# Kernel optimization log

Measured on AMD Instinct MI355X. Metric: run time of the kernel, lower is better.

Reference implementation:

```python
import jax, jax.numpy as jnp
import numpy as np

DIM = 96
D_STATE = 16
EXPAND = 2
D_INNER = EXPAND * DIM
DT_RANK = (DIM + 15) // 16  # 6
B, H, W = 2, 64, 64
K = 4  # scan directions


def _ln(x, w, b, eps=1e-5):
    mu = x.mean(-1, keepdims=True)
    var = x.var(-1, keepdims=True)
    return (x - mu) / jnp.sqrt(var + eps) * w + b


def setup_inputs() -> dict:
    key = jax.random.key(0)
    ks = jax.random.split(key, 10)
    f = jnp.float32
    x = jax.random.normal(ks[0], (B, H, W, DIM), dtype=f)
    y = jax.random.normal(ks[1], (B, H, W, DIM), dtype=f)
    inp = {
        'x': x,
        'y': y,
        'ln_w': jnp.ones((DIM,), f),
        'ln_b': jnp.zeros((DIM,), f),
        'in_proj_w': jax.random.normal(ks[2], (2 * D_INNER, DIM), f) * 0.05,
        'conv_w': jax.random.normal(ks[3], (D_INNER, 1, 3, 3), f) * 0.1,
        'conv_b': jnp.zeros((D_INNER,), f),
        'x_proj_w': jax.random.normal(ks[4], (K, DT_RANK + 2 * D_STATE, D_INNER), f) * 0.05,
        'dt_w': jax.random.normal(ks[5], (K, D_INNER, DT_RANK), f) * 0.1,
        'dt_b': jax.random.normal(ks[6], (K, D_INNER), f) * 0.1,
        'A_log': jnp.broadcast_to(jnp.log(jnp.arange(1, D_STATE + 1, dtype=f)), (K, D_INNER, D_STATE)),
        'Ds': jnp.ones((K, D_INNER), f),
        'out_norm_w': jnp.ones((D_INNER,), f),
        'out_norm_b': jnp.zeros((D_INNER,), f),
        'out_proj_w': jax.random.normal(ks[7], (DIM, D_INNER), f) * 0.05,
    }
    return inp


def _fwd(x, y, ln_w, ln_b, in_proj_w, conv_w, conv_b, x_proj_w, dt_w, dt_b,
         A_log, Ds, out_norm_w, out_norm_b, out_proj_w):
    Bsz, Hh, Ww, C = x.shape
    Din = conv_w.shape[0]
    N = A_log.shape[-1]
    R = dt_w.shape[-1]
    L = Hh * Ww

    diff = jnp.abs(x - y)                       # TemporalSpectrumBlock abs-diff
    h = _ln(diff, ln_w, ln_b)                   # VSSBlock ln_1
    xz = h @ in_proj_w.T                        # (B,H,W,2*Din)
    xm, z = jnp.split(xz, 2, axis=-1)
    xm = xm.transpose(0, 3, 1, 2)               # (B,Din,H,W)
    xm = jax.lax.conv_general_dilated(
        xm, conv_w, (1, 1), 'SAME', feature_group_count=Din,
        dimension_numbers=('NCHW', 'OIHW', 'NCHW')) + conv_b[None, :, None, None]
    xm = jax.nn.silu(xm)

    # 4-directional sequences (B,4,Din,L)
    x0 = xm.reshape(Bsz, Din, L)
    x1 = xm.transpose(0, 1, 3, 2).reshape(Bsz, Din, L)
    xs = jnp.stack([x0, x1], axis=1)
    xs = jnp.concatenate([xs, jnp.flip(xs, axis=-1)], axis=1)

    x_dbl = jnp.einsum('bkdl,kcd->bkcl', xs, x_proj_w)
    dts, Bs, Cs = jnp.split(x_dbl, [R, R + N], axis=2)   # (B,4,R,L),(B,4,N,L),(B,4,N,L)
    dts = jnp.einsum('bkrl,kdr->bkdl', dts, dt_w)
    delta = jax.nn.softplus(dts + dt_b[None, :, :, None])  # (B,4,Din,L)

    A = -jnp.exp(A_log)                                    # (4,Din,N)
    dA = jnp.exp(delta[..., None] * A[None, :, :, None, :])          # (B,4,Din,L,N)
    dBu = delta[..., None] * Bs.transpose(0, 1, 3, 2)[:, :, None] * xs[..., None]

    dA_t = dA.transpose(3, 0, 1, 2, 4)    # (L,B,4,Din,N)
    dBu_t = dBu.transpose(3, 0, 1, 2, 4)
    C_t = Cs.transpose(3, 0, 1, 2)        # (L,B,4,N)
    h0 = jnp.zeros((Bsz, 4, Din, N), dtype=x.dtype)

    def step(hc, inp):
        a, bu, c = inp
        hc = a * hc + bu
        yv = jnp.einsum('bkdn,bkn->bkd', hc, c)
        return hc, yv

    _, ys = jax.lax.scan(step, h0, (dA_t, dBu_t, C_t))    # (L,B,4,Din)
    ys = ys.transpose(1, 2, 3, 0)                          # (B,4,Din,L)
    out_y = ys + Ds[None, :, :, None] * xs

    inv_y = jnp.flip(out_y[:, 2:4], axis=-1)
    wh_y = out_y[:, 1].reshape(Bsz, Din, Ww, Hh).transpose(0, 1, 3, 2).reshape(Bsz, Din, L)
    invwh_y = inv_y[:, 1].reshape(Bsz, Din, Ww, Hh).transpose(0, 1, 3, 2).reshape(Bsz, Din, L)
    yc = out_y[:, 0] + inv_y[:, 0] + wh_y + invwh_y        # (B,Din,L)
    yc = yc.transpose(0, 2, 1).reshape(Bsz, Hh, Ww, Din)

    yn = _ln(yc, out_norm_w, out_norm_b)
    out = (yn * jax.nn.silu(z)) @ out_proj_w.T
    return diff + out                                      # residual around the block


def reference(x, y, ln_w, ln_b, in_proj_w, conv_w, conv_b, x_proj_w, dt_w, dt_b,
              A_log, Ds, out_norm_w, out_norm_b, out_proj_w):
    return _fwd(x, y, ln_w, ln_b, in_proj_w, conv_w, conv_b, x_proj_w, dt_w, dt_b,
                A_log, Ds, out_norm_w, out_norm_b, out_proj_w)
```

## Files before the change

kernel.cpp:

```cpp
#include <hip/hip_runtime.h>
#include <math.h>

#define DIMC 96
#define DIN  192
#define NST  16
#define RNK  6
#define KD   4
#define HH   64
#define WWD  64
#define LL   4096
#define BB   2
#define NC   128
#define CH   32
#define CPK  48

__device__ __forceinline__ int pos_of(int k, int l) {
    int t = ((l & 63) << 6) | (l >> 6);
    switch (k) {
        case 0: return l;
        case 1: return t;
        case 2: return LL - 1 - l;
        default: return ((((LL-1-l) & 63) << 6) | ((LL-1-l) >> 6));
    }
}

__device__ __forceinline__ float silu_f(float v) {
    return v / (1.f + __expf(-v));
}

__global__ __launch_bounds__(1024) void k1_ln_inproj(
    const float* __restrict__ x, const float* __restrict__ y,
    const float* __restrict__ lnw, const float* __restrict__ lnb,
    const float* __restrict__ Win, const float* __restrict__ Wout,
    const float* __restrict__ xpw,
    float* __restrict__ diff, float* __restrict__ xm, float* __restrict__ zbuf,
    float* __restrict__ wT3, float* __restrict__ WoutT)
{
    __shared__ float hT[96*65];
    __shared__ float ps1[16*64], ps2[16*64];
    __shared__ float mus[64], rss[64];
    int t = threadIdx.x;
    int ptile = blockIdx.x >> 1, cgrp = blockIdx.x & 1;
    int p0 = ptile*64;

    {
        int gid = blockIdx.x*1024 + t;
        if (gid < KD*192*CPK) {
            int kk = gid / (192*CPK); int rem = gid - kk*192*CPK;
            int j = rem / CPK, c = rem - j*CPK;
            float v = 0.f;
            if (c < 16)       v = xpw[((size_t)kk*(RNK+2*NST) + RNK + c)*DIN + j];
            else if (c < 32)  v = xpw[((size_t)kk*(RNK+2*NST) + RNK + NST + (c-16))*DIN + j];
            else if (c < 38)  v = xpw[((size_t)kk*(RNK+2*NST) + (c-32))*DIN + j];
            wT3[gid] = v;
        } else if (gid < KD*192*CPK + 192*96) {
            int i = gid - KD*192*CPK;
            int j = i / 96, o = i - j*96;
            WoutT[i] = Wout[o*192 + j];
        }
    }

    #pragma unroll
    for (int s = 0; s < 6; s++) {
        int i = t + 1024*s;
        float v = fabsf(x[(size_t)p0*96 + i] - y[(size_t)p0*96 + i]);
        if (cgrp == 0) diff[(size_t)p0*96 + i] = v;
        int pos = i / 96, ch = i - pos*96;
        hT[ch*65 + pos] = v;
    }
    __syncthreads();
    {
        int pos = t & 63, part = t >> 6;
        float s1 = 0.f, s2 = 0.f;
        #pragma unroll
        for (int m = 0; m < 6; m++) {
            float v = hT[(part*6 + m)*65 + pos];
            s1 += v; s2 += v*v;
        }
        ps1[part*64 + pos] = s1; ps2[part*64 + pos] = s2;
    }
    __syncthreads();
    if (t < 64) {
        float S1 = 0.f, S2 = 0.f;
        #pragma unroll
        for (int i = 0; i < 16; i++) { S1 += ps1[i*64 + t]; S2 += ps2[i*64 + t]; }
        float mu = S1 * (1.f/96.f);
        float var = S2 * (1.f/96.f) - mu*mu;
        mus[t] = mu; rss[t] = rsqrtf(var + 1e-5f);
    }
    __syncthreads();
    #pragma unroll
    for (int s = 0; s < 6; s++) {
        int i = t + 1024*s;
        int pos = i / 96, ch = i - pos*96;
        hT[ch*65 + pos] = (hT[ch*65 + pos] - mus[pos]) * rss[pos] * lnw[ch] + lnb[ch];
    }
    __syncthreads();

    int w = __builtin_amdgcn_readfirstlane(t >> 6);
    int lane = t & 63;
    int c0 = cgrp*192 + w*12;
    const float* wrows = Win + (size_t)c0*96;
    float acc[12];
    #pragma unroll
    for (int cc = 0; cc < 12; cc++) acc[cc] = 0.f;
    #pragma unroll 2
    for (int j = 0; j < 96; j++) {
        float u = hT[j*65 + lane];
        #pragma unroll
        for (int cc = 0; cc < 12; cc++) acc[cc] += u * wrows[cc*96 + j];
    }
    size_t p = (size_t)(p0 + lane);
    float* dst = (c0 < 192) ? (xm + p*192 + c0) : (zbuf + p*192 + (c0 - 192));
    #pragma unroll
    for (int q = 0; q < 3; q++)
        *(float4*)&dst[4*q] = make_float4(acc[4*q], acc[4*q+1], acc[4*q+2], acc[4*q+3]);
}

__global__ __launch_bounds__(192) void k2_conv(
    const float* __restrict__ xm, const float* __restrict__ cw,
    const float* __restrict__ cb, float* __restrict__ xconv)
{
    int p = blockIdx.x;
    int d = threadIdx.x;
    int b = p >> 12;
    int l = p & (LL - 1);
    int hh = l >> 6, ww = l & 63;
    float acc = cb[d];
    const float* wd = cw + d*9;
    #pragma unroll
    for (int di = -1; di <= 1; di++) {
        int h2 = hh + di;
        if ((unsigned)h2 < HH) {
            #pragma unroll
            for (int dj = -1; dj <= 1; dj++) {
                int w2 = ww + dj;
                if ((unsigned)w2 < WWD)
                    acc += wd[(di+1)*3 + (dj+1)] * xm[((size_t)b*LL + h2*WWD + w2)*DIN + d];
            }
        }
    }
    xconv[(size_t)p*DIN + d] = silu_f(acc);
}

__global__ __launch_bounds__(512) void k3_xproj(
    const float* __restrict__ xconv, const float* __restrict__ wT3,
    float* __restrict__ XDK)
{
    __shared__ float uT[64*192];
    int t = threadIdx.x;
    int ptile = blockIdx.x >> 1, wgrp = blockIdx.x & 1;
    int p0 = ptile*64;

    #pragma unroll
    for (int s = 0; s < 24; s++) {
        int i = t + 512*s;
        int pos = i / 192, ch = i - pos*192;
        int c4 = (ch >> 2) ^ (pos & 7);
        uT[pos*192 + (c4 << 2) + (ch & 3)] = xconv[(size_t)(p0 + pos)*192 + ch];
    }
    __syncthreads();

    int w = __builtin_amdgcn_readfirstlane(t >> 6);
    int slot = wgrp*8 + w;
    int k = slot >> 2, cq = slot & 3;
    int lane = t & 63;
    int c0 = cq*12;
    const float* wp = wT3 + (size_t)k*192*CPK + c0;
    const float* urow = uT + lane*192;
    int sw = lane & 7;
    float acc[12];
    #pragma unroll
    for (int cc = 0; cc < 12; cc++) acc[cc] = 0.f;
    #pragma unroll 4
    for (int j4 = 0; j4 < 48; j4++) {
        float4 u4 = *(const float4*)&urow[((j4 ^ sw) << 2)];
        const float* wrow = wp + (j4*4)*CPK;
        #pragma unroll
        for (int cc = 0; cc < 12; cc++) acc[cc] += u4.x * wrow[cc];
        #pragma unroll
        for (int cc = 0; cc < 12; cc++) acc[cc] += u4.y * wrow[CPK + cc];
        #pragma unroll
        for (int cc = 0; cc < 12; cc++) acc[cc] += u4.z * wrow[2*CPK + cc];
        #pragma unroll
        for (int cc = 0; cc < 12; cc++) acc[cc] += u4.w * wrow[3*CPK + cc];
    }
    int p = p0 + lane;
    int b = p >> 12;
    int s = p & (LL - 1);
    int ts = ((s & 63) << 6) | (s >> 6);
    int l;
    switch (k) {
        case 0: l = s; break;
        case 1: l = ts; break;
        case 2: l = LL - 1 - s; break;
        default: l = LL - 1 - ts; break;
    }
    float* dst = XDK + ((size_t)(b*KD + k)*LL + l)*CPK + c0;
    #pragma unroll
    for (int q = 0; q < 3; q++)
        *(float4*)&dst[4*q] = make_float4(acc[4*q], acc[4*q+1], acc[4*q+2], acc[4*q+3]);
}

__global__ __launch_bounds__(192) void k4_scanA(
    const float* __restrict__ xconv, const float* __restrict__ XDK,
    const float* __restrict__ dtw, const float* __restrict__ dtb,
    const float* __restrict__ A_log,
    float* __restrict__ Sarr, float* __restrict__ Q)
{
    int blk = blockIdx.x;
    int c  = blk & (NC - 1);
    int bk = blk >> 7;
    int k  = bk & 3;
    int b  = bk >> 2;
    int d  = threadIdx.x;
    float dw[RNK];
    #pragma unroll
    for (int r = 0; r < RNK; r++) dw[r] = dtw[((size_t)k*DIN + d)*RNK + r];
    float bias = dtb[k*DIN + d];
    float A[NST];
    #pragma unroll
    for (int n = 0; n < NST; n++) A[n] = -__expf(A_log[((size_t)k*DIN + d)*NST + n]);
    bool fastA = true;
    #pragma unroll
    for (int n = 1; n < NST; n++)
        fastA = fastA && (fabsf(A[n] - (float)(n+1)*A[0]) <= 1e-4f*(float)(n+1));

    float h[NST];
    #pragma unroll
    for (int n = 0; n < NST; n++) h[n] = 0.f;
    float S = 0.f;

    size_t rb = ((size_t)bk*LL + c*CH)*CPK;
    if (fastA) {
        #pragma unroll 2
        for (int step = 0; step < CH; step++) {
            const float* rec = XDK + rb + step*CPK;
            float dl = bias;
            #pragma unroll
            for (int r = 0; r < RNK; r++) dl += rec[32 + r] * dw[r];
            dl = (dl > 20.f) ? dl : __logf(1.f + __expf(dl));
            int l = c*CH + step;
            float uu = xconv[((size_t)b*LL + pos_of(k, l))*DIN + d];
            float du = dl * uu;
            S += dl;
            float e1 = __expf(dl * A[0]);
            float e2 = e1*e1, e4 = e2*e2;
            float p0 = e1, p1 = e2, p2 = e2*e1, p3 = e4;
            #pragma unroll
            for (int g = 0; g < 4; g++) {
                h[4*g+0] = p0*h[4*g+0] + du*rec[4*g+0];
                h[4*g+1] = p1*h[4*g+1] + du*rec[4*g+1];
                h[4*g+2] = p2*h[4*g+2] + du*rec[4*g+2];
                h[4*g+3] = p3*h[4*g+3] + du*rec[4*g+3];
                if (g < 3) { p0 *= e4; p1 *= e4; p2 *= e4; p3 *= e4; }
            }
        }
    } else {
        #pragma unroll 2
        for (int step = 0; step < CH; step++) {
            const float* rec = XDK + rb + step*CPK;
            float dl = bias;
            #pragma unroll
            for (int r = 0; r < RNK; r++) dl += rec[32 + r] * dw[r];
            dl = (dl > 20.f) ? dl : __logf(1.f + __expf(dl));
            int l = c*CH + step;
            float uu = xconv[((size_t)b*LL + pos_of(k, l))*DIN + d];
            float du = dl * uu;
            S += dl;
            #pragma unroll
            for (int n = 0; n < NST; n++) {
                float a = __expf(dl * A[n]);
                h[n] = a*h[n] + du*rec[n];
            }
        }
    }
    Sarr[(size_t)blk*DIN + d] = S;
    size_t qb = (size_t)blk*NST*DIN + d;
    #pragma unroll
    for (int n = 0; n < NST; n++) Q[qb + n*DIN] = h[n];
}

__global__ __launch_bounds__(256) void k5_scanB(
    const float* __restrict__ A_log, const float* __restrict__ Sarr,
    float* __restrict__ Q)
{
    int idx = blockIdx.x*256 + threadIdx.x;
    if (idx >= BB*KD*NST*DIN) return;
    int d = idx % DIN;
    int rest = idx / DIN;
    int n = rest % NST; rest /= NST;
    int k = rest & 3;
    int b = rest >> 2;
    int bk = b*KD + k;
    float A = -__expf(A_log[((size_t)k*DIN + d)*NST + n]);
    size_t qstride = (size_t)NST*DIN;
    size_t qbase = (size_t)bk*NC*qstride + n*DIN + d;
    size_t sbase = (size_t)bk*NC*DIN + d;
    float h = 0.f;
    #pragma unroll 4
    for (int c = 0; c < NC; c++) {
        float s = Sarr[sbase + c*DIN];
        float q = Q[qbase + c*qstride];
        Q[qbase + c*qstride] = h;
        h = __expf(A*s)*h + q;
    }
}

__global__ __launch_bounds__(192) void k6_scanC(
    const float* __restrict__ xconv, const float* __restrict__ XDK,
    const float* __restrict__ dtw, const float* __restrict__ dtb,
    const float* __restrict__ A_log, const float* __restrict__ Ds,
    const float* __restrict__ Q, float* __restrict__ outy)
{
    int blk = blockIdx.x;
    int c  = blk & (NC - 1);
    int bk = blk >> 7;
    int k  = bk & 3;
    int b  = bk >> 2;
    int d  = threadIdx.x;
    float dw[RNK];
    #pragma unroll
    for (int r = 0; r < RNK; r++) dw[r] = dtw[((size_t)k*DIN + d)*RNK + r];
    float bias = dtb[k*DIN + d];
    float A[NST];
    #pragma unroll
    for (int n = 0; n < NST; n++) A[n] = -__expf(A_log[((size_t)k*DIN + d)*NST + n]);
    bool fastA = true;
    #pragma unroll
    for (int n = 1; n < NST; n++)
        fastA = fastA && (fabsf(A[n] - (float)(n+1)*A[0]) <= 1e-4f*(float)(n+1));
    float h[NST];
    size_t qb = (size_t)blk*NST*DIN + d;
    #pragma unroll
    for (int n = 0; n < NST; n++) h[n] = Q[qb + n*DIN];
    float Dv = Ds[k*DIN + d];

    size_t rb = ((size_t)bk*LL + c*CH)*CPK;
    if (fastA) {
        #pragma unroll 2
        for (int step = 0; step < CH; step++) {
            const float* rec = XDK + rb + step*CPK;
            float dl = bias;
            #pragma unroll
            for (int r = 0; r < RNK; r++) dl += rec[32 + r] * dw[r];
            dl = (dl > 20.f) ? dl : __logf(1.f + __expf(dl));
            int l = c*CH + step;
            int sp = pos_of(k, l);
            float uu = xconv[((size_t)b*LL + sp)*DIN + d];
            float du = dl * uu;
            float e1 = __expf(dl * A[0]);
            float e2 = e1*e1, e4 = e2*e2;
            float p0 = e1, p1 = e2, p2 = e2*e1, p3 = e4;
            float yv = 0.f;
            #pragma unroll
            for (int g = 0; g < 4; g++) {
                h[4*g+0] = p0*h[4*g+0] + du*rec[4*g+0];
                h[4*g+1] = p1*h[4*g+1] + du*rec[4*g+1];
                h[4*g+2] = p2*h[4*g+2] + du*rec[4*g+2];
                h[4*g+3] = p3*h[4*g+3] + du*rec[4*g+3];
                yv += h[4*g+0]*rec[16+4*g+0] + h[4*g+1]*rec[16+4*g+1]
                    + h[4*g+2]*rec[16+4*g+2] + h[4*g+3]*rec[16+4*g+3];
                if (g < 3) { p0 *= e4; p1 *= e4; p2 *= e4; p3 *= e4; }
            }
            outy[((size_t)bk*LL + sp)*DIN + d] = yv + Dv*uu;
        }
    } else {
        #pragma unroll 2
        for (int step = 0; step < CH; step++) {
            const float* rec = XDK + rb + step*CPK;
            float dl = bias;
            #pragma unroll
            for (int r = 0; r < RNK; r++) dl += rec[32 + r] * dw[r];
            dl = (dl > 20.f) ? dl : __logf(1.f + __expf(dl));
            int l = c*CH + step;
            int sp = pos_of(k, l);
            float uu = xconv[((size_t)b*LL + sp)*DIN + d];
            float du = dl * uu;
            float yv = 0.f;
            #pragma unroll
            for (int n = 0; n < NST; n++) {
                float a = __expf(dl * A[n]);
                h[n] = a*h[n] + du*rec[n];
                yv += h[n] * rec[16 + n];
            }
            outy[((size_t)bk*LL + sp)*DIN + d] = yv + Dv*uu;
        }
    }
}

__global__ __launch_bounds__(512) void k7_out(
    const float* __restrict__ outy, const float* __restrict__ zbuf,
    const float* __restrict__ diff, const float* __restrict__ onw,
    const float* __restrict__ onb, const float* __restrict__ WoutT,
    float* __restrict__ out)
{
    __shared__ float gT[192*65];
    __shared__ float ps1[8*64], ps2[8*64];
    __shared__ float mus[64], rss[64];
    int t = threadIdx.x;
    int ptile = blockIdx.x >> 1, chalf = blockIdx.x & 1;
    int p0 = ptile*64;
    int b = p0 >> 12;
    int l0 = p0 & (LL - 1);
    const size_t seg = (size_t)LL*DIN;
    size_t base = ((size_t)(b*KD)*LL + l0)*DIN;

    #pragma unroll
    for (int s = 0; s < 24; s++) {
        int i = t + 512*s;
        float yc = outy[base + i] + outy[base + seg + i]
                 + outy[base + 2*seg + i] + outy[base + 3*seg + i];
        int pos = i / 192, ch = i - pos*192;
        gT[ch*65 + pos] = yc;
    }
    __syncthreads();
    {
        int pos = t & 63, part = t >> 6;
        float s1 = 0.f, s2 = 0.f;
        #pragma unroll
        for (int m = 0; m < 24; m++) {
            float v = gT[(part*24 + m)*65 + pos];
            s1 += v; s2 += v*v;
        }
        ps1[part*64 + pos] = s1; ps2[part*64 + pos] = s2;
    }
    __syncthreads();
    if (t < 64) {
        float S1 = 0.f, S2 = 0.f;
        #pragma unroll
        for (int i = 0; i < 8; i++) { S1 += ps1[i*64 + t]; S2 += ps2[i*64 + t]; }
        float mu = S1 * (1.f/192.f);
        float var = S2 * (1.f/192.f) - mu*mu;
        mus[t] = mu; rss[t] = rsqrtf(var + 1e-5f);
    }
    __syncthreads();
    #pragma unroll
    for (int s = 0; s < 24; s++) {
        int i = t + 512*s;
        int pos = i / 192, ch = i - pos*192;
        float v = gT[ch*65 + pos];
        float yn = (v - mus[pos]) * rss[pos] * onw[ch] + onb[ch];
        float z = zbuf[(size_t)p0*DIN + i];
        gT[ch*65 + pos] = yn * silu_f(z);
    }
    __syncthreads();

    int w = __builtin_amdgcn_readfirstlane(t >> 6);
    int lane = t & 63;
    int c0 = chalf*48 + w*6;
    const float* wp = WoutT + c0;
    float acc[6];
    #pragma unroll
    for (int cc = 0; cc < 6; cc++) acc[cc] = 0.f;
    #pragma unroll 4
    for (int j = 0; j < 192; j++) {
        float u = gT[j*65 + lane];
        const float* wrow = wp + j*96;
        #pragma unroll
        for (int cc = 0; cc < 6; cc++) acc[cc] += u * wrow[cc];
    }
    size_t p = (size_t)(p0 + lane);
    #pragma unroll
    for (int q = 0; q < 3; q++) {
        float2 dv = *(const float2*)&diff[p*96 + c0 + 2*q];
        *(float2*)&out[p*96 + c0 + 2*q] =
            make_float2(acc[2*q] + dv.x, acc[2*q+1] + dv.y);
    }
}

extern "C" void kernel_launch(void* const* d_in, const int* in_sizes, int n_in,
                              void* d_out, int out_size, void* d_ws, size_t ws_size,
                              hipStream_t stream)
{
    const float* x       = (const float*)d_in[0];
    const float* y       = (const float*)d_in[1];
    const float* ln_w    = (const float*)d_in[2];
    const float* ln_b    = (const float*)d_in[3];
    const float* in_proj = (const float*)d_in[4];
    const float* conv_w  = (const float*)d_in[5];
    const float* conv_b  = (const float*)d_in[6];
    const float* x_proj  = (const float*)d_in[7];
    const float* dt_w    = (const float*)d_in[8];
    const float* dt_b    = (const float*)d_in[9];
    const float* A_log   = (const float*)d_in[10];
    const float* Ds      = (const float*)d_in[11];
    const float* onw     = (const float*)d_in[12];
    const float* onb     = (const float*)d_in[13];
    const float* out_w   = (const float*)d_in[14];
    float* out = (float*)d_out;

    float* ws    = (float*)d_ws;
    float* diff  = ws;
    float* zbuf  = diff  + 786432;
    float* xm    = zbuf  + 1572864;
    float* xconv = xm    + 1572864;
    float* XDK   = xconv + 1572864;
    float* outy  = XDK   + 1572864;
    float* Qbuf  = outy  + 6291456;
    float* Sarr  = Qbuf  + 6291456;
    float* WoutT = Sarr  + 393216;
    float* wT3   = WoutT + 18432;

    const int BL = BB * LL;

    hipLaunchKernelGGL(k1_ln_inproj, dim3(BL/64*2), dim3(1024), 0, stream,
                       x, y, ln_w, ln_b, in_proj, out_w, x_proj,
                       diff, xm, zbuf, wT3, WoutT);
    hipLaunchKernelGGL(k2_conv, dim3(BL), dim3(DIN), 0, stream,
                       xm, conv_w, conv_b, xconv);
    hipLaunchKernelGGL(k3_xproj, dim3(BL/64*2), dim3(512), 0, stream,
                       xconv, wT3, XDK);
    hipLaunchKernelGGL(k4_scanA, dim3(BB*KD*NC), dim3(DIN), 0, stream,
                       xconv, XDK, dt_w, dt_b, A_log, Sarr, Qbuf);
    hipLaunchKernelGGL(k5_scanB, dim3((BB*KD*NST*DIN + 255)/256), dim3(256), 0, stream,
                       A_log, Sarr, Qbuf);
    hipLaunchKernelGGL(k6_scanC, dim3(BB*KD*NC), dim3(DIN), 0, stream,
                       xconv, XDK, dt_w, dt_b, A_log, Ds, Qbuf, outy);
    hipLaunchKernelGGL(k7_out, dim3(BL/64*2), dim3(512), 0, stream,
                       outy, zbuf, diff, onw, onb, WoutT, out);
}
```

Measured before the change: 254.9 us.

## Accumulate four scan directions into one buffer via atomicAdd

The scan output kernel now atomically adds each direction's result into a single combined (B,L,Din) buffer instead of writing four separate per-direction buffers. The extra blocks of the chunk-carry kernel zero that buffer first. The output kernel then reads one value per element instead of summing four. This cuts global write and read traffic and workspace size, at the cost of float atomics with up to four-way contention per address and a non-deterministic summation order.

Measured after the change: 246.1 us, median of 2. -3.5%, faster.

```diff
diff --git a/kernel.cpp b/kernel.cpp
--- a/kernel.cpp
+++ b/kernel.cpp
@@ -13,6 +13,8 @@
 #define NC   128
 #define CH   32
 #define CPK  48
+#define SCANB_BLKS 96
+#define ZERO_BLKS  384
 
 __device__ __forceinline__ int pos_of(int k, int l) {
     int t = ((l & 63) << 6) | (l >> 6);
@@ -283,8 +285,16 @@
 
 __global__ __launch_bounds__(256) void k5_scanB(
     const float* __restrict__ A_log, const float* __restrict__ Sarr,
-    float* __restrict__ Q)
-{
+    float* __restrict__ Q, float* __restrict__ outc)
+{
+    if (blockIdx.x >= SCANB_BLKS) {
+        int zi = (blockIdx.x - SCANB_BLKS)*256 + threadIdx.x;
+        float4* o4 = (float4*)outc;
+        float4 z4 = make_float4(0.f, 0.f, 0.f, 0.f);
+        #pragma unroll
+        for (int j = 0; j < 4; j++) o4[zi + j*98304] = z4;
+        return;
+    }
     int idx = blockIdx.x*256 + threadIdx.x;
     if (idx >= BB*KD*NST*DIN) return;
     int d = idx % DIN;
@@ -311,7 +321,7 @@
     const float* __restrict__ xconv, const float* __restrict__ XDK,
     const float* __restrict__ dtw, const float* __restrict__ dtb,
     const float* __restrict__ A_log, const float* __restrict__ Ds,
-    const float* __restrict__ Q, float* __restrict__ outy)
+    const float* __restrict__ Q, float* __restrict__ outc)
 {
     int blk = blockIdx.x;
     int c  = blk & (NC - 1);
@@ -363,7 +373,7 @@
                     + h[4*g+2]*rec[16+4*g+2] + h[4*g+3]*rec[16+4*g+3];
                 if (g < 3) { p0 *= e4; p1 *= e4; p2 *= e4; p3 *= e4; }
             }
-            outy[((size_t)bk*LL + sp)*DIN + d] = yv + Dv*uu;
+            atomicAdd(&outc[((size_t)b*LL + sp)*DIN + d], yv + Dv*uu);
         }
     } else {
         #pragma unroll 2
@@ -384,13 +394,13 @@
                 h[n] = a*h[n] + du*rec[n];
                 yv += h[n] * rec[16 + n];
             }
-            outy[((size_t)bk*LL + sp)*DIN + d] = yv + Dv*uu;
+            atomicAdd(&outc[((size_t)b*LL + sp)*DIN + d], yv + Dv*uu);
         }
     }
 }
 
 __global__ __launch_bounds__(512) void k7_out(
-    const float* __restrict__ outy, const float* __restrict__ zbuf,
+    const float* __restrict__ outc, const float* __restrict__ zbuf,
     const float* __restrict__ diff, const float* __restrict__ onw,
     const float* __restrict__ onb, const float* __restrict__ WoutT,
     float* __restrict__ out)
@@ -401,16 +411,11 @@
     int t = threadIdx.x;
     int ptile = blockIdx.x >> 1, chalf = blockIdx.x & 1;
     int p0 = ptile*64;
-    int b = p0 >> 12;
-    int l0 = p0 & (LL - 1);
-    const size_t seg = (size_t)LL*DIN;
-    size_t base = ((size_t)(b*KD)*LL + l0)*DIN;
 
     #pragma unroll
     for (int s = 0; s < 24; s++) {
         int i = t + 512*s;
-        float yc = outy[base + i] + outy[base + seg + i]
-                 + outy[base + 2*seg + i] + outy[base + 3*seg + i];
+        float yc = outc[(size_t)p0*DIN + i];
         int pos = i / 192, ch = i - pos*192;
         gT[ch*65 + pos] = yc;
     }
@@ -496,10 +501,10 @@
     float* xm    = zbuf  + 1572864;
     float* xconv = xm    + 1572864;
     float* XDK   = xconv + 1572864;
-    float* outy  = XDK   + 1572864;
-    float* Qbuf  = outy  + 6291456;
-    float* Sarr  = Qbuf  + 6291456;
-    float* WoutT = Sarr  + 393216;
+    float* outc  = XDK   + 1572864;
+    float* Qbuf  = outc  + 1572864;
+    float* Sarr  = Qbuf  + 3145728;
+    float* WoutT = Sarr  + 196608;
     float* wT3   = WoutT + 18432;
 
     const int BL = BB * LL;
@@ -513,10 +518,10 @@
                        xconv, wT3, XDK);
     hipLaunchKernelGGL(k4_scanA, dim3(BB*KD*NC), dim3(DIN), 0, stream,
                        xconv, XDK, dt_w, dt_b, A_log, Sarr, Qbuf);
-    hipLaunchKernelGGL(k5_scanB, dim3((BB*KD*NST*DIN + 255)/256), dim3(256), 0, stream,
-                       A_log, Sarr, Qbuf);
+    hipLaunchKernelGGL(k5_scanB, dim3(SCANB_BLKS + ZERO_BLKS), dim3(256), 0, stream,
+                       A_log, Sarr, Qbuf, outc);
     hipLaunchKernelGGL(k6_scanC, dim3(BB*KD*NC), dim3(DIN), 0, stream,
-                       xconv, XDK, dt_w, dt_b, A_log, Ds, Qbuf, outy);
+                       xconv, XDK, dt_w, dt_b, A_log, Ds, Qbuf, outc);
     hipLaunchKernelGGL(k7_out, dim3(BL/64*2), dim3(512), 0, stream,
-                       outy, zbuf, diff, onw, onb, WoutT, out);
-}
+                       outc, zbuf, diff, onw, onb, WoutT, out);
+}
```
